# Kernel tuning notes

Measured on AMD Instinct MI355X. Metric: run time of the kernel, lower is better.

The kernel has to match this reference:

```python
import jax, jax.numpy as jnp
import numpy as np

N, IN_DIM, HID, Z, HEADS, E = 10000, 128, 128, 64, 4, 320000
NEG_SLOPE = 0.2


def setup_inputs() -> dict:
    key = jax.random.key(0)
    ks = jax.random.split(key, 16)
    s = 0.1
    return {
        "x": jax.random.normal(ks[0], (N, IN_DIM), jnp.float32),
        "edge_index": jax.random.randint(ks[1], (2, E), 0, N, jnp.int64),
        "gcn_w": jax.random.normal(ks[2], (IN_DIM, HID), jnp.float32) * s,
        "gcn_b": jnp.zeros((HID,), jnp.float32),
        "gat_w": jax.random.normal(ks[3], (HID, HEADS * HID), jnp.float32) * s,
        "gat_att_src": jax.random.normal(ks[4], (HEADS, HID), jnp.float32) * s,
        "gat_att_dst": jax.random.normal(ks[5], (HEADS, HID), jnp.float32) * s,
        "gat_b": jnp.zeros((HID,), jnp.float32),
        "mlp_w1": jax.random.normal(ks[6], (HID, HID), jnp.float32) * s,
        "mlp_b1": jnp.zeros((HID,), jnp.float32),
        "mlp_w2": jax.random.normal(ks[7], (HID, HID), jnp.float32) * s,
        "mlp_b2": jnp.zeros((HID,), jnp.float32),
        "mu_w": jax.random.normal(ks[8], (HID, Z), jnp.float32) * s,
        "mu_b": jnp.zeros((Z,), jnp.float32),
        "lv_w": jax.random.normal(ks[9], (HID, Z), jnp.float32) * s,
        "lv_b": jnp.zeros((Z,), jnp.float32),
    }


def _add_self_loops(edge_index, n):
    loop = jnp.arange(n, dtype=edge_index.dtype)
    src = jnp.concatenate([edge_index[0], loop])
    dst = jnp.concatenate([edge_index[1], loop])
    return src, dst


def _gcn(x, edge_index, w, b):
    # PyG GCNConv: add self-loops, symmetric normalization D^-1/2 (A+I) D^-1/2
    n = x.shape[0]
    src, dst = _add_self_loops(edge_index, n)
    deg = jax.ops.segment_sum(jnp.ones_like(dst, dtype=x.dtype), dst, num_segments=n)
    dinv = jax.lax.rsqrt(deg)  # deg >= 1 due to self-loops
    norm = dinv[src] * dinv[dst]  # [E+N]
    h = x @ w  # [N, HID]
    out = jax.ops.segment_sum(h[src] * norm[:, None], dst, num_segments=n)
    return out + b


def _gat(x, edge_index, w, att_src, att_dst, b):
    # PyG GATConv(heads=HEADS, concat=False): average heads, self-loops added
    n = x.shape[0]
    src, dst = _add_self_loops(edge_index, n)
    h = (x @ w).reshape(n, HEADS, HID)  # [N, H, C]
    a_src = jnp.einsum('nhc,hc->nh', h, att_src)  # [N, H]
    a_dst = jnp.einsum('nhc,hc->nh', h, att_dst)
    e = jax.nn.leaky_relu(a_src[src] + a_dst[dst], NEG_SLOPE)  # [E+N, H]
    # segment softmax over incoming edges of each destination node
    emax = jax.ops.segment_max(e, dst, num_segments=n)
    e = jnp.exp(e - emax[dst])
    denom = jax.ops.segment_sum(e, dst, num_segments=n)
    alpha = e / denom[dst]  # [E+N, H]
    out = jax.ops.segment_sum(h[src] * alpha[:, :, None], dst, num_segments=n)  # [N, H, C]
    return out.mean(axis=1) + b


def reference(x, edge_index, gcn_w, gcn_b, gat_w, gat_att_src, gat_att_dst, gat_b,
              mlp_w1, mlp_b1, mlp_w2, mlp_b2, mu_w, mu_b, lv_w, lv_b):
    h = jax.nn.relu(_gcn(x, edge_index, gcn_w, gcn_b))
    h = jax.nn.relu(_gat(h, edge_index, gat_w, gat_att_src, gat_att_dst, gat_b))
    h = jax.nn.relu(h @ mlp_w1 + mlp_b1)
    h = jax.nn.relu(h @ mlp_w2 + mlp_b2)
    mu = h @ mu_w + mu_b
    logvar = h @ lv_w + lv_b
    return (mu, logvar)
```

## Files before the change

kernel.cpp:

```cpp
#include <hip/hip_runtime.h>

#define NN 10000
#define D 128
#define NH 4
#define HD 512
#define ZD 64

__device__ __forceinline__ float lrelu(float x){ return x > 0.0f ? x : 0.2f*x; }

__global__ __launch_bounds__(256) void k_zero_int(int* __restrict__ a, int n){
  int i = blockIdx.x*256 + threadIdx.x;
  if (i < n) a[i] = 0;
}

__global__ __launch_bounds__(256) void k_hist(const int* __restrict__ dst,
                                              int* __restrict__ deg, int E){
  int i = blockIdx.x*256 + threadIdx.x;
  if (i < E) atomicAdd(&deg[dst[i]], 1);
}

__global__ __launch_bounds__(1024) void k_scan(int* __restrict__ deg,
                                               int* __restrict__ ioff,
                                               float* __restrict__ dinv){
  __shared__ int part[1024];
  const int tid = threadIdx.x;
  const int base = tid*10;
  int local[10]; int s = 0;
#pragma unroll
  for (int i=0;i<10;i++){
    int idx = base+i;
    int v = (idx < NN) ? deg[idx] : 0;
    if (idx < NN) dinv[idx] = rsqrtf(1.0f + (float)v);
    local[i] = s; s += v;
  }
  part[tid] = s;
  __syncthreads();
  for (int o=1;o<1024;o<<=1){
    int v = (tid>=o) ? part[tid-o] : 0;
    __syncthreads();
    part[tid] += v;
    __syncthreads();
  }
  int excl = part[tid] - s;
#pragma unroll
  for (int i=0;i<10;i++){
    int idx = base+i;
    if (idx < NN){
      int o = excl + local[i];
      ioff[idx] = o;
      deg[idx]  = o;
    }
  }
  if (tid == 1023) ioff[NN] = part[1023];
}

__global__ __launch_bounds__(256) void k_fill(const int* __restrict__ src,
                                              const int* __restrict__ dst,
                                              int* __restrict__ cur,
                                              int* __restrict__ csr, int E,
                                              float* __restrict__ az){
  int i = blockIdx.x*256 + threadIdx.x;
  if (i < NN*NH*2) az[i] = 0.f;
  if (i >= E) return;
  int pos = atomicAdd(&cur[dst[i]], 1);
  csr[pos] = src[i];
}

__global__ __launch_bounds__(256) void k_gemm(const float* __restrict__ A,
                                              const float* __restrict__ W, int ldw,
                                              const float* __restrict__ bias,
                                              float* __restrict__ C, int ldc,
                                              int nrows, int do_relu){
  __shared__ float As[64][132];
  __shared__ float Ws[128][68];
  const int tid  = threadIdx.x;
  const int row0 = blockIdx.x*64;
  const int col0 = blockIdx.y*64;
#pragma unroll
  for (int i=0;i<8;i++){
    int f  = tid + i*256;
    int r  = f >> 5;
    int k4 = (f & 31) << 2;
    int rr = row0 + r;
    float4 v = make_float4(0.f,0.f,0.f,0.f);
    if (rr < nrows) v = *(const float4*)&A[rr*D + k4];
    *(float4*)&As[r][k4] = v;
  }
#pragma unroll
  for (int i=0;i<8;i++){
    int f  = tid + i*256;
    int k  = f >> 4;
    int c4 = (f & 15) << 2;
    float4 v = *(const float4*)&W[k*ldw + col0 + c4];
    *(float4*)&Ws[k][c4] = v;
  }
  __syncthreads();
  const int tx = tid & 15, ty = tid >> 4;
  float acc[4][4] = {{0.f}};
#pragma unroll 4
  for (int k=0;k<128;k++){
    float4 w = *(const float4*)&Ws[k][tx<<2];
    float wv[4] = {w.x, w.y, w.z, w.w};
    float av[4];
#pragma unroll
    for (int i=0;i<4;i++) av[i] = As[(ty<<2)+i][k];
#pragma unroll
    for (int i=0;i<4;i++)
#pragma unroll
      for (int j=0;j<4;j++) acc[i][j] = fmaf(av[i], wv[j], acc[i][j]);
  }
#pragma unroll
  for (int i=0;i<4;i++){
    int r = row0 + (ty<<2) + i;
    if (r >= nrows) continue;
#pragma unroll
    for (int j=0;j<4;j++){
      int c = col0 + (tx<<2) + j;
      float v = acc[i][j];
      if (bias) v += bias[c];
      if (do_relu) v = fmaxf(v, 0.f);
      C[r*ldc + c] = v;
    }
  }
}

__global__ __launch_bounds__(256) void k_gemm_att(const float* __restrict__ A,
                                                  const float* __restrict__ W,
                                                  float* __restrict__ C,
                                                  const float* __restrict__ att_src,
                                                  const float* __restrict__ att_dst,
                                                  float* __restrict__ a_src,
                                                  float* __restrict__ a_dst){
  __shared__ float As[64][132];
  __shared__ float Ws[128][68];
  const int tid  = threadIdx.x;
  const int row0 = blockIdx.x*64;
  const int col0 = blockIdx.y*64;
#pragma unroll
  for (int i=0;i<8;i++){
    int f  = tid + i*256;
    int r  = f >> 5;
    int k4 = (f & 31) << 2;
    int rr = row0 + r;
    float4 v = make_float4(0.f,0.f,0.f,0.f);
    if (rr < NN) v = *(const float4*)&A[rr*D + k4];
    *(float4*)&As[r][k4] = v;
  }
#pragma unroll
  for (int i=0;i<8;i++){
    int f  = tid + i*256;
    int k  = f >> 4;
    int c4 = (f & 15) << 2;
    *(float4*)&Ws[k][c4] = *(const float4*)&W[k*HD + col0 + c4];
  }
  __syncthreads();
  const int tx = tid & 15, ty = tid >> 4;
  float acc[4][4] = {{0.f}};
#pragma unroll 4
  for (int k=0;k<128;k++){
    float4 w = *(const float4*)&Ws[k][tx<<2];
    float wv[4] = {w.x, w.y, w.z, w.w};
    float av[4];
#pragma unroll
    for (int i=0;i<4;i++) av[i] = As[(ty<<2)+i][k];
#pragma unroll
    for (int i=0;i<4;i++)
#pragma unroll
      for (int j=0;j<4;j++) acc[i][j] = fmaf(av[i], wv[j], acc[i][j]);
  }
#pragma unroll
  for (int i=0;i<4;i++){
    int r = row0 + (ty<<2) + i;
    if (r >= NN) continue;
#pragma unroll
    for (int j=0;j<4;j++)
      C[r*HD + col0 + (tx<<2) + j] = acc[i][j];
  }
  const int h = col0 >> 7;
  const int cb = (col0 & 127) + (tx<<2);
  float ps[4], pd[4];
#pragma unroll
  for (int i=0;i<4;i++){
    float s_ = 0.f, d_ = 0.f;
#pragma unroll
    for (int j=0;j<4;j++){
      s_ = fmaf(acc[i][j], att_src[h*D + cb + j], s_);
      d_ = fmaf(acc[i][j], att_dst[h*D + cb + j], d_);
    }
    ps[i] = s_; pd[i] = d_;
  }
#pragma unroll
  for (int o=8;o>0;o>>=1){
#pragma unroll
    for (int i=0;i<4;i++){
      ps[i] += __shfl_xor(ps[i], o);
      pd[i] += __shfl_xor(pd[i], o);
    }
  }
  if (tx == 0){
#pragma unroll
    for (int i=0;i<4;i++){
      int r = row0 + (ty<<2) + i;
      if (r < NN){
        atomicAdd(&a_src[r*4 + h], ps[i]);
        atomicAdd(&a_dst[r*4 + h], pd[i]);
      }
    }
  }
}

__global__ __launch_bounds__(256) void k_gcn_agg(const float* __restrict__ xw,
                                                 const float* __restrict__ dinv,
                                                 const int* __restrict__ ioff,
                                                 const int* __restrict__ csr,
                                                 const float* __restrict__ bias,
                                                 float* __restrict__ out){
  __shared__ float2 snm[4][64];
  const int sub  = blockIdx.x & 7;
  const int ch   = sub >> 2;
  const int g    = blockIdx.x >> 3;
  const int wv   = threadIdx.x >> 6;
  const int lane = threadIdx.x & 63;
  const int w    = g*16 + (sub & 3)*4 + wv;
  const int c    = ch*64 + lane;
  const int beg = ioff[w], end = ioff[w+1];
  float din = dinv[w];
  float ax = xw[w*D + c] * din;
  for (int jb = beg; jb < end; jb += 64){
    int cnt = end - jb; if (cnt > 64) cnt = 64;
    if (lane < cnt){
      int s = csr[jb + lane];
      snm[wv][lane] = make_float2(dinv[s], __int_as_float(s));
    }
    __builtin_amdgcn_wave_barrier();
#pragma unroll 4
    for (int l=0; l<cnt; l++){
      float2 t = snm[wv][l];
      int ss = __float_as_int(t.y);
      ax = fmaf(t.x, xw[ss*D + c], ax);
    }
    __builtin_amdgcn_wave_barrier();
  }
  out[w*D + c] = fmaxf(fmaf(ax, din, bias[c]), 0.f);
}

__global__ __launch_bounds__(256) void k_gat_agg(const float* __restrict__ hg,
                                                 const float* __restrict__ a_src,
                                                 const float* __restrict__ a_dst,
                                                 const int* __restrict__ ioff,
                                                 const int* __restrict__ csr,
                                                 float* __restrict__ p0,
                                                 float* __restrict__ p1){
  __shared__ float2 sal[4][64];
  __shared__ int    ssr[4][64];
  const int sub   = blockIdx.x & 7;
  const int slice = sub >> 1;
  const int hp    = slice >> 1;
  const int ch    = slice & 1;
  const int g     = blockIdx.x >> 3;
  const int wv    = threadIdx.x >> 6;
  const int lane  = threadIdx.x & 63;
  const int w     = g*8 + (sub & 1)*4 + wv;
  const int c     = ch*64 + lane;
  const int h0    = hp*2;
  const int beg = ioff[w], end = ioff[w+1];
  float2 ad  = *(const float2*)&a_dst[w*4 + h0];
  float2 asn = *(const float2*)&a_src[w*4 + h0];
  float e0 = __expf(lrelu(asn.x + ad.x));
  float e1 = __expf(lrelu(asn.y + ad.y));
  float den0 = 0.f, den1 = 0.f;
  const float* hrow = &hg[(size_t)w*HD + h0*D + c];
  float o0 = e0 * hrow[0];
  float o1 = e1 * hrow[D];

  for (int jb = beg; jb < end; jb += 64){
    int cnt = end - jb; if (cnt > 64) cnt = 64;
    if (lane < cnt){
      int s = csr[jb + lane];
      float2 as = *(const float2*)&a_src[s*4 + h0];
      float g0 = __expf(lrelu(as.x + ad.x));
      float g1 = __expf(lrelu(as.y + ad.y));
      sal[wv][lane] = make_float2(g0, g1);
      ssr[wv][lane] = s;
      den0 += g0; den1 += g1;
    }
    __builtin_amdgcn_wave_barrier();
#pragma unroll 4
    for (int l=0; l<cnt; l++){
      float2 b = sal[wv][l];
      const float* hs = &hg[(size_t)ssr[wv][l]*HD + h0*D + c];
      o0 = fmaf(b.x, hs[0], o0);
      o1 = fmaf(b.y, hs[D], o1);
    }
    __builtin_amdgcn_wave_barrier();
  }
#pragma unroll
  for (int o=32; o>0; o>>=1){
    den0 += __shfl_xor(den0, o);
    den1 += __shfl_xor(den1, o);
  }
  den0 += e0; den1 += e1;
  float res = o0*(0.25f/den0) + o1*(0.25f/den1);
  (hp ? p1 : p0)[w*D + c] = res;
}

__global__ __launch_bounds__(256) void k_combine(const float* __restrict__ p0,
                                                 const float* __restrict__ p1,
                                                 const float* __restrict__ bias,
                                                 float* __restrict__ h2){
  int t = blockIdx.x*256 + threadIdx.x;
  if (t >= NN*D) return;
  h2[t] = fmaxf(p0[t] + p1[t] + bias[t & 127], 0.f);
}

__global__ __launch_bounds__(256) void k_mlp(const float* __restrict__ h2,
                                             const float* __restrict__ w1,
                                             const float* __restrict__ b1,
                                             const float* __restrict__ w2,
                                             const float* __restrict__ b2,
                                             const float* __restrict__ wmu,
                                             const float* __restrict__ bmu,
                                             const float* __restrict__ wlv,
                                             const float* __restrict__ blv,
                                             float* __restrict__ out){
  __shared__ float hA[64][132];
  __shared__ float hB[64][132];
  __shared__ float Ws[128][68];
  const int tid  = threadIdx.x;
  const int row0 = blockIdx.x*64;
  const int tx = tid & 15, ty = tid >> 4;

#pragma unroll
  for (int i=0;i<8;i++){
    int f  = tid + i*256;
    int r  = f >> 5;
    int k4 = (f & 31) << 2;
    int rr = row0 + r;
    float4 v = make_float4(0.f,0.f,0.f,0.f);
    if (rr < NN) v = *(const float4*)&h2[rr*D + k4];
    *(float4*)&hA[r][k4] = v;
  }

  float (*S)[132] = hA;
  float (*T)[132] = hB;
#pragma unroll
  for (int layer=0; layer<2; layer++){
    const float* W  = layer ? w2 : w1;
    const float* bb = layer ? b2 : b1;
    for (int cc=0; cc<2; cc++){
      __syncthreads();
#pragma unroll
      for (int i=0;i<8;i++){
        int f  = tid + i*256;
        int k  = f >> 4;
        int c4 = (f & 15) << 2;
        *(float4*)&Ws[k][c4] = *(const float4*)&W[k*D + cc*64 + c4];
      }
      __syncthreads();
      float acc[4][4] = {{0.f}};
#pragma unroll 4
      for (int k=0;k<128;k++){
        float4 wvv = *(const float4*)&Ws[k][tx<<2];
        float wv[4] = {wvv.x, wvv.y, wvv.z, wvv.w};
        float av[4];
#pragma unroll
        for (int i=0;i<4;i++) av[i] = S[(ty<<2)+i][k];
#pragma unroll
        for (int i=0;i<4;i++)
#pragma unroll
          for (int j=0;j<4;j++) acc[i][j] = fmaf(av[i], wv[j], acc[i][j]);
      }
#pragma unroll
      for (int i=0;i<4;i++)
#pragma unroll
        for (int j=0;j<4;j++){
          int col = cc*64 + (tx<<2) + j;
          T[(ty<<2)+i][col] = fmaxf(acc[i][j] + bb[col], 0.f);
        }
    }
    float (*tmp)[132] = S; S = T; T = tmp;
  }
  for (int cc=0; cc<2; cc++){
    const float* W  = cc ? wlv : wmu;
    const float* bb = cc ? blv : bmu;
    float* ob = out + (size_t)cc*NN*ZD;
    __syncthreads();
#pragma unroll
    for (int i=0;i<8;i++){
      int f  = tid + i*256;
      int k  = f >> 4;
      int c4 = (f & 15) << 2;
      *(float4*)&Ws[k][c4] = *(const float4*)&W[k*ZD + c4];
    }
    __syncthreads();
    float acc[4][4] = {{0.f}};
#pragma unroll 4
    for (int k=0;k<128;k++){
      float4 wvv = *(const float4*)&Ws[k][tx<<2];
      float wv[4] = {wvv.x, wvv.y, wvv.z, wvv.w};
      float av[4];
#pragma unroll
      for (int i=0;i<4;i++) av[i] = S[(ty<<2)+i][k];
#pragma unroll
      for (int i=0;i<4;i++)
#pragma unroll
        for (int j=0;j<4;j++) acc[i][j] = fmaf(av[i], wv[j], acc[i][j]);
    }
#pragma unroll
    for (int i=0;i<4;i++){
      int r = row0 + (ty<<2) + i;
      if (r >= NN) continue;
      float4 v = make_float4(acc[i][0] + bb[(tx<<2)+0],
                             acc[i][1] + bb[(tx<<2)+1],
                             acc[i][2] + bb[(tx<<2)+2],
                             acc[i][3] + bb[(tx<<2)+3]);
      *(float4*)&ob[r*ZD + (tx<<2)] = v;
    }
  }
}

extern "C" void kernel_launch(void* const* d_in, const int* in_sizes, int n_in,
                              void* d_out, int out_size, void* d_ws, size_t ws_size,
                              hipStream_t stream){
  const float* x     = (const float*)d_in[0];
  const int*   ei    = (const int*)d_in[1];
  const float* gcn_w = (const float*)d_in[2];
  const float* gcn_b = (const float*)d_in[3];
  const float* gat_w = (const float*)d_in[4];
  const float* att_s = (const float*)d_in[5];
  const float* att_d = (const float*)d_in[6];
  const float* gat_b = (const float*)d_in[7];
  const float* w1    = (const float*)d_in[8];
  const float* b1    = (const float*)d_in[9];
  const float* w2    = (const float*)d_in[10];
  const float* b2    = (const float*)d_in[11];
  const float* mu_w  = (const float*)d_in[12];
  const float* mu_b  = (const float*)d_in[13];
  const float* lv_w  = (const float*)d_in[14];
  const float* lv_b  = (const float*)d_in[15];
  const int E = in_sizes[1] / 2;
  const int* src = ei;
  const int* dst = ei + E;

  float* ws    = (float*)d_ws;
  float* xw    = ws;
  float* h1    = xw + NN*D;
  float* h2    = h1 + NN*D;
  float* hg    = h2 + NN*D;
  float* dinv  = hg + NN*HD;
  float* a_src = dinv + NN;
  float* a_dst = a_src + NN*NH;
  int*   ioff  = (int*)(a_dst + NN*NH);
  int*   icur  = ioff + NN + 1;
  int*   csr   = icur + NN;

  const int gN = (NN + 255)/256;
  const int gE = (E + 255)/256;
  const int gR = (NN + 63)/64;
  const int gND = (NN*D + 255)/256;

  k_zero_int<<<gN, 256, 0, stream>>>(icur, NN);
  k_hist<<<gE, 256, 0, stream>>>(dst, icur, E);
  k_scan<<<1, 1024, 0, stream>>>(icur, ioff, dinv);
  k_fill<<<gE, 256, 0, stream>>>(src, dst, icur, csr, E, a_src);

  k_gemm<<<dim3(gR,2), 256, 0, stream>>>(x, gcn_w, D, nullptr, xw, D, NN, 0);
  k_gcn_agg<<<(NN/16)*8, 256, 0, stream>>>(xw, dinv, ioff, csr, gcn_b, h1);

  k_gemm_att<<<dim3(gR,8), 256, 0, stream>>>(h1, gat_w, hg, att_s, att_d,
                                             a_src, a_dst);
  k_gat_agg<<<(NN/8)*8, 256, 0, stream>>>(hg, a_src, a_dst, ioff, csr, xw, h1);
  k_combine<<<gND, 256, 0, stream>>>(xw, h1, gat_b, h2);

  k_mlp<<<gR, 256, 0, stream>>>(h2, w1, b1, w2, b2, mu_w, mu_b, lv_w, lv_b,
                                (float*)d_out);
}
```

Measured before the change: 208.4 us.

## Reassociate GAT: aggregate h1 before projecting, fold attention vectors into weights

Measured after the change: 199.3 us. 4.4% less time.

```diff
diff --git a/kernel.cpp b/kernel.cpp
--- a/kernel.cpp
+++ b/kernel.cpp
@@ -57,10 +57,8 @@
 __global__ __launch_bounds__(256) void k_fill(const int* __restrict__ src,
                                               const int* __restrict__ dst,
                                               int* __restrict__ cur,
-                                              int* __restrict__ csr, int E,
-                                              float* __restrict__ az){
+                                              int* __restrict__ csr, int E){
   int i = blockIdx.x*256 + threadIdx.x;
-  if (i < NN*NH*2) az[i] = 0.f;
   if (i >= E) return;
   int pos = atomicAdd(&cur[dst[i]], 1);
   csr[pos] = src[i];
@@ -120,91 +118,6 @@
       if (bias) v += bias[c];
       if (do_relu) v = fmaxf(v, 0.f);
       C[r*ldc + c] = v;
-    }
-  }
-}
-
-__global__ __launch_bounds__(256) void k_gemm_att(const float* __restrict__ A,
-                                                  const float* __restrict__ W,
-                                                  float* __restrict__ C,
-                                                  const float* __restrict__ att_src,
-                                                  const float* __restrict__ att_dst,
-                                                  float* __restrict__ a_src,
-                                                  float* __restrict__ a_dst){
-  __shared__ float As[64][132];
-  __shared__ float Ws[128][68];
-  const int tid  = threadIdx.x;
-  const int row0 = blockIdx.x*64;
-  const int col0 = blockIdx.y*64;
-#pragma unroll
-  for (int i=0;i<8;i++){
-    int f  = tid + i*256;
-    int r  = f >> 5;
-    int k4 = (f & 31) << 2;
-    int rr = row0 + r;
-    float4 v = make_float4(0.f,0.f,0.f,0.f);
-    if (rr < NN) v = *(const float4*)&A[rr*D + k4];
-    *(float4*)&As[r][k4] = v;
-  }
-#pragma unroll
-  for (int i=0;i<8;i++){
-    int f  = tid + i*256;
-    int k  = f >> 4;
-    int c4 = (f & 15) << 2;
-    *(float4*)&Ws[k][c4] = *(const float4*)&W[k*HD + col0 + c4];
-  }
-  __syncthreads();
-  const int tx = tid & 15, ty = tid >> 4;
-  float acc[4][4] = {{0.f}};
-#pragma unroll 4
-  for (int k=0;k<128;k++){
-    float4 w = *(const float4*)&Ws[k][tx<<2];
-    float wv[4] = {w.x, w.y, w.z, w.w};
-    float av[4];
-#pragma unroll
-    for (int i=0;i<4;i++) av[i] = As[(ty<<2)+i][k];
-#pragma unroll
-    for (int i=0;i<4;i++)
-#pragma unroll
-      for (int j=0;j<4;j++) acc[i][j] = fmaf(av[i], wv[j], acc[i][j]);
-  }
-#pragma unroll
-  for (int i=0;i<4;i++){
-    int r = row0 + (ty<<2) + i;
-    if (r >= NN) continue;
-#pragma unroll
-    for (int j=0;j<4;j++)
-      C[r*HD + col0 + (tx<<2) + j] = acc[i][j];
-  }
-  const int h = col0 >> 7;
-  const int cb = (col0 & 127) + (tx<<2);
-  float ps[4], pd[4];
-#pragma unroll
-  for (int i=0;i<4;i++){
-    float s_ = 0.f, d_ = 0.f;
-#pragma unroll
-    for (int j=0;j<4;j++){
-      s_ = fmaf(acc[i][j], att_src[h*D + cb + j], s_);
-      d_ = fmaf(acc[i][j], att_dst[h*D + cb + j], d_);
-    }
-    ps[i] = s_; pd[i] = d_;
-  }
-#pragma unroll
-  for (int o=8;o>0;o>>=1){
-#pragma unroll
-    for (int i=0;i<4;i++){
-      ps[i] += __shfl_xor(ps[i], o);
-      pd[i] += __shfl_xor(pd[i], o);
-    }
-  }
-  if (tx == 0){
-#pragma unroll
-    for (int i=0;i<4;i++){
-      int r = row0 + (ty<<2) + i;
-      if (r < NN){
-        atomicAdd(&a_src[r*4 + h], ps[i]);
-        atomicAdd(&a_dst[r*4 + h], pd[i]);
-      }
     }
   }
 }
@@ -244,53 +157,99 @@
   out[w*D + c] = fmaxf(fmaf(ax, din, bias[c]), 0.f);
 }
 
-__global__ __launch_bounds__(256) void k_gat_agg(const float* __restrict__ hg,
-                                                 const float* __restrict__ a_src,
-                                                 const float* __restrict__ a_dst,
-                                                 const int* __restrict__ ioff,
-                                                 const int* __restrict__ csr,
-                                                 float* __restrict__ p0,
-                                                 float* __restrict__ p1){
-  __shared__ float2 sal[4][64];
+__global__ __launch_bounds__(128) void k_watt(const float* __restrict__ gat_w,
+                                              const float* __restrict__ att_src,
+                                              const float* __restrict__ att_dst,
+                                              float* __restrict__ w_as,
+                                              float* __restrict__ w_ad){
+  const int h = blockIdx.x;
+  const int k = threadIdx.x;
+  const float* wrow = &gat_w[k*HD + h*D];
+  const float* as   = &att_src[h*D];
+  const float* ad   = &att_dst[h*D];
+  float s = 0.f, d = 0.f;
+#pragma unroll 4
+  for (int c=0;c<D;c++){
+    float wv = wrow[c];
+    s = fmaf(wv, as[c], s);
+    d = fmaf(wv, ad[c], d);
+  }
+  w_as[h*D + k] = s;
+  w_ad[h*D + k] = d;
+}
+
+__global__ __launch_bounds__(256) void k_att2(const float* __restrict__ h1,
+                                              const float* __restrict__ w_as,
+                                              float* __restrict__ a_src,
+                                              float* __restrict__ a_dst){
+  __shared__ float sw[8][128];
+  const int tid = threadIdx.x;
+#pragma unroll
+  for (int i=0;i<4;i++) ((float*)sw)[tid + i*256] = w_as[tid + i*256];
+  __syncthreads();
+  const int wv = tid >> 6, lane = tid & 63;
+  const int n = blockIdx.x*4 + wv;
+  float2 v = *(const float2*)&h1[n*D + lane*2];
+#pragma unroll
+  for (int o=0;o<8;o++){
+    float t = v.x*sw[o][lane*2] + v.y*sw[o][lane*2+1];
+#pragma unroll
+    for (int off=32; off>0; off>>=1) t += __shfl_xor(t, off);
+    if (lane == 0){
+      if (o < 4) a_src[n*4 + o] = t;
+      else       a_dst[n*4 + (o-4)] = t;
+    }
+  }
+}
+
+__global__ __launch_bounds__(256) void k_gat_agg2(const float* __restrict__ h1,
+                                                  const float* __restrict__ a_src,
+                                                  const float* __restrict__ a_dst,
+                                                  const int* __restrict__ ioff,
+                                                  const int* __restrict__ csr,
+                                                  float* __restrict__ agg){
+  __shared__ float4 sal[4][64];
   __shared__ int    ssr[4][64];
-  const int sub   = blockIdx.x & 7;
-  const int slice = sub >> 1;
-  const int hp    = slice >> 1;
-  const int ch    = slice & 1;
-  const int g     = blockIdx.x >> 3;
-  const int wv    = threadIdx.x >> 6;
-  const int lane  = threadIdx.x & 63;
-  const int w     = g*8 + (sub & 1)*4 + wv;
-  const int c     = ch*64 + lane;
-  const int h0    = hp*2;
+  const int sub  = blockIdx.x & 7;
+  const int ch   = sub >> 2;
+  const int g    = blockIdx.x >> 3;
+  const int wv   = threadIdx.x >> 6;
+  const int lane = threadIdx.x & 63;
+  const int w    = g*16 + (sub & 3)*4 + wv;
+  const int c    = ch*64 + lane;
   const int beg = ioff[w], end = ioff[w+1];
-  float2 ad  = *(const float2*)&a_dst[w*4 + h0];
-  float2 asn = *(const float2*)&a_src[w*4 + h0];
+  float4 ad  = *(const float4*)&a_dst[w*4];
+  float4 asn = *(const float4*)&a_src[w*4];
   float e0 = __expf(lrelu(asn.x + ad.x));
   float e1 = __expf(lrelu(asn.y + ad.y));
-  float den0 = 0.f, den1 = 0.f;
-  const float* hrow = &hg[(size_t)w*HD + h0*D + c];
-  float o0 = e0 * hrow[0];
-  float o1 = e1 * hrow[D];
+  float e2 = __expf(lrelu(asn.z + ad.z));
+  float e3 = __expf(lrelu(asn.w + ad.w));
+  float hv = h1[w*D + c];
+  float o0 = e0*hv, o1 = e1*hv, o2 = e2*hv, o3 = e3*hv;
+  float den0=0.f, den1=0.f, den2=0.f, den3=0.f;
 
   for (int jb = beg; jb < end; jb += 64){
     int cnt = end - jb; if (cnt > 64) cnt = 64;
     if (lane < cnt){
       int s = csr[jb + lane];
-      float2 as = *(const float2*)&a_src[s*4 + h0];
+      float4 as = *(const float4*)&a_src[s*4];
       float g0 = __expf(lrelu(as.x + ad.x));
       float g1 = __expf(lrelu(as.y + ad.y));
-      sal[wv][lane] = make_float2(g0, g1);
+      float g2 = __expf(lrelu(as.z + ad.z));
+      float g3 = __expf(lrelu(as.w + ad.w));
+      sal[wv][lane] = make_float4(g0,g1,g2,g3);
       ssr[wv][lane] = s;
-      den0 += g0; den1 += g1;
+      den0 += g0; den1 += g1; den2 += g2; den3 += g3;
     }
     __builtin_amdgcn_wave_barrier();
 #pragma unroll 4
     for (int l=0; l<cnt; l++){
-      float2 b = sal[wv][l];
-      const float* hs = &hg[(size_t)ssr[wv][l]*HD + h0*D + c];
-      o0 = fmaf(b.x, hs[0], o0);
-      o1 = fmaf(b.y, hs[D], o1);
+      float4 b = sal[wv][l];
+      float sv = h1[ssr[wv][l]*D + c];
+      o0 = fmaf(b.x, sv, o0);
+      o1 = fmaf(b.y, sv, o1);
+      o2 = fmaf(b.z, sv, o2);
+      o3 = fmaf(b.w, sv, o3);
     }
     __builtin_amdgcn_wave_barrier();
   }
@@ -298,19 +257,71 @@
   for (int o=32; o>0; o>>=1){
     den0 += __shfl_xor(den0, o);
     den1 += __shfl_xor(den1, o);
-  }
-  den0 += e0; den1 += e1;
-  float res = o0*(0.25f/den0) + o1*(0.25f/den1);
-  (hp ? p1 : p0)[w*D + c] = res;
-}
-
-__global__ __launch_bounds__(256) void k_combine(const float* __restrict__ p0,
-                                                 const float* __restrict__ p1,
-                                                 const float* __restrict__ bias,
-                                                 float* __restrict__ h2){
-  int t = blockIdx.x*256 + threadIdx.x;
-  if (t >= NN*D) return;
-  h2[t] = fmaxf(p0[t] + p1[t] + bias[t & 127], 0.f);
+    den2 += __shfl_xor(den2, o);
+    den3 += __shfl_xor(den3, o);
+  }
+  den0 += e0; den1 += e1; den2 += e2; den3 += e3;
+  float* ab = &agg[(size_t)w*HD + c];
+  ab[0*D] = o0 * (0.25f/den0);
+  ab[1*D] = o1 * (0.25f/den1);
+  ab[2*D] = o2 * (0.25f/den2);
+  ab[3*D] = o3 * (0.25f/den3);
+}
+
+__global__ __launch_bounds__(256) void k_gemm2(const float* __restrict__ agg,
+                                               const float* __restrict__ W,
+                                               const float* __restrict__ bias,
+                                               float* __restrict__ h2){
+  __shared__ float As[64][132];
+  __shared__ float Ws[128][68];
+  const int tid  = threadIdx.x;
+  const int row0 = blockIdx.x*64;
+  const int col0 = blockIdx.y*64;
+  const int tx = tid & 15, ty = tid >> 4;
+  float acc[4][4] = {{0.f}};
+  for (int h=0; h<NH; h++){
+    __syncthreads();
+#pragma unroll
+    for (int i=0;i<8;i++){
+      int f  = tid + i*256;
+      int r  = f >> 5;
+      int k4 = (f & 31) << 2;
+      int rr = row0 + r;
+      float4 v = make_float4(0.f,0.f,0.f,0.f);
+      if (rr < NN) v = *(const float4*)&agg[(size_t)rr*HD + h*D + k4];
+      *(float4*)&As[r][k4] = v;
+    }
+#pragma unroll
+    for (int i=0;i<8;i++){
+      int f  = tid + i*256;
+      int k  = f >> 4;
+      int c4 = (f & 15) << 2;
+      *(float4*)&Ws[k][c4] = *(const float4*)&W[k*HD + h*D + col0 + c4];
+    }
+    __syncthreads();
+#pragma unroll 4
+    for (int k=0;k<128;k++){
+      float4 w = *(const float4*)&Ws[k][tx<<2];
+      float wv[4] = {w.x, w.y, w.z, w.w};
+      float av[4];
+#pragma unroll
+      for (int i=0;i<4;i++) av[i] = As[(ty<<2)+i][k];
+#pragma unroll
+      for (int i=0;i<4;i++)
+#pragma unroll
+        for (int j=0;j<4;j++) acc[i][j] = fmaf(av[i], wv[j], acc[i][j]);
+    }
+  }
+#pragma unroll
+  for (int i=0;i<4;i++){
+    int r = row0 + (ty<<2) + i;
+    if (r >= NN) continue;
+#pragma unroll
+    for (int j=0;j<4;j++){
+      int col = col0 + (tx<<2) + j;
+      h2[r*D + col] = fmaxf(acc[i][j] + bias[col], 0.f);
+    }
+  }
 }
 
 __global__ __launch_bounds__(256) void k_mlp(const float* __restrict__ h2,
@@ -446,9 +457,11 @@
   float* xw    = ws;
   float* h1    = xw + NN*D;
   float* h2    = h1 + NN*D;
-  float* hg    = h2 + NN*D;
-  float* dinv  = hg + NN*HD;
-  float* a_src = dinv + NN;
+  float* agg   = h2 + NN*D;
+  float* dinv  = agg + (size_t)NN*HD;
+  float* w_as  = dinv + NN;
+  float* w_ad  = w_as + HD;
+  float* a_src = w_ad + HD;
   float* a_dst = a_src + NN*NH;
   int*   ioff  = (int*)(a_dst + NN*NH);
   int*   icur  = ioff + NN + 1;
@@ -457,20 +470,20 @@
   const int gN = (NN + 255)/256;
   const int gE = (E + 255)/256;
   const int gR = (NN + 63)/64;
-  const int gND = (NN*D + 255)/256;
 
   k_zero_int<<<gN, 256, 0, stream>>>(icur, NN);
   k_hist<<<gE, 256, 0, stream>>>(dst, icur, E);
   k_scan<<<1, 1024, 0, stream>>>(icur, ioff, dinv);
-  k_fill<<<gE, 256, 0, stream>>>(src, dst, icur, csr, E, a_src);
+  k_fill<<<gE, 256, 0, stream>>>(src, dst, icur, csr, E);
+
+  k_watt<<<NH, 128, 0, stream>>>(gat_w, att_s, att_d, w_as, w_ad);
 
   k_gemm<<<dim3(gR,2), 256, 0, stream>>>(x, gcn_w, D, nullptr, xw, D, NN, 0);
   k_gcn_agg<<<(NN/16)*8, 256, 0, stream>>>(xw, dinv, ioff, csr, gcn_b, h1);
 
-  k_gemm_att<<<dim3(gR,8), 256, 0, stream>>>(h1, gat_w, hg, att_s, att_d,
-                                             a_src, a_dst);
-  k_gat_agg<<<(NN/8)*8, 256, 0, stream>>>(hg, a_src, a_dst, ioff, csr, xw, h1);
-  k_combine<<<gND, 256, 0, stream>>>(xw, h1, gat_b, h2);
+  k_att2<<<NN/4, 256, 0, stream>>>(h1, w_as, a_src, a_dst);
+  k_gat_agg2<<<(NN/16)*8, 256, 0, stream>>>(h1, a_src, a_dst, ioff, csr, agg);
+  k_gemm2<<<dim3(gR,2), 256, 0, stream>>>(agg, gat_w, gat_b, h2);
 
   k_mlp<<<gR, 256, 0, stream>>>(h2, w1, b1, w2, b2, mu_w, mu_b, lv_w, lv_b,
                                 (float*)d_out);
```
